# Optimization experiments

Hardware: AMD Instinct MI355X
Metric: run time of the kernel (lower is better)

The kernel has to match this reference:

```python
import jax, jax.numpy as jnp
import numpy as np

N_HEADS = 16

def setup_inputs() -> dict:
    key = jax.random.key(0)
    ks = jax.random.split(key, 9)
    B, S, E = 2, 2048, 1024
    s = 1.0 / np.sqrt(E)
    return {
        "x":  jax.random.normal(ks[0], (B, S, E), jnp.float32),
        "Wq": jax.random.normal(ks[1], (E, E), jnp.float32) * s,
        "bq": jax.random.normal(ks[2], (E,), jnp.float32) * 0.01,
        "Wk": jax.random.normal(ks[3], (E, E), jnp.float32) * s,
        "bk": jax.random.normal(ks[4], (E,), jnp.float32) * 0.01,
        "Wv": jax.random.normal(ks[5], (E, E), jnp.float32) * s,
        "bv": jax.random.normal(ks[6], (E,), jnp.float32) * 0.01,
        "Wo": jax.random.normal(ks[7], (E, E), jnp.float32) * s,
        "bo": jax.random.normal(ks[8], (E,), jnp.float32) * 0.01,
    }

def reference(x, Wq, bq, Wk, bk, Wv, bv, Wo, bo):
    B, S, E = x.shape
    H = N_HEADS
    D = E // H
    # torch nn.Linear: y = x @ W.T + b
    q = (x @ Wq.T + bq).reshape(B, S, H, D)
    k = (x @ Wk.T + bk).reshape(B, S, H, D)
    v = (x @ Wv.T + bv).reshape(B, S, H, D)
    # scores: [B, H, Q, K]
    scores = jnp.einsum('bqnd,bknd->bnqk', q, k) / jnp.sqrt(jnp.float32(D))
    # NOTE: original code softmaxes over dim=1 == the HEADS axis (faithful quirk)
    attn = jax.nn.softmax(scores, axis=1)
    # dropout p=0 -> identity
    out = jnp.einsum('bnqk,bknd->bnqd', attn, v)      # [B, H, Q, D]
    out = out.transpose(0, 2, 1, 3).reshape(B, S, E)  # [B, S, E]
    return out @ Wo.T + bo
```

## Files before the change

### kernel.cpp

```cpp
#include <hip/hip_runtime.h>
#include <cstddef>
#include <cstdint>

#define BATCH 2
#define S_LEN 2048
#define E_DIM 1024
#define NH    16
#define HD    64
#define M_ROWS (BATCH * S_LEN)

#define QSCALE 0.18033688011112042f

typedef unsigned short u16;
typedef short     bf16x8 __attribute__((ext_vector_type(8)));
typedef _Float16  f16x8  __attribute__((ext_vector_type(8)));
typedef __fp16    h16x2  __attribute__((ext_vector_type(2)));
typedef float     f32x4  __attribute__((ext_vector_type(4)));

__device__ __forceinline__ u16 f2bf(float f) {
    union { float f; unsigned u; } v; v.f = f;
    unsigned r = v.u + 0x7fffu + ((v.u >> 16) & 1u);
    return (u16)(r >> 16);
}
__device__ __forceinline__ float bf2f(u16 h) {
    union { unsigned u; float f; } v; v.u = ((unsigned)h) << 16;
    return v.f;
}

__device__ __forceinline__ void load_lds16(const u16* g, u16* l) {
    __builtin_amdgcn_global_load_lds(
        (const __attribute__((address_space(1))) unsigned int*)g,
        (__attribute__((address_space(3))) unsigned int*)l, 16, 0, 0);
}

__global__ void cvt_bf16(const float* __restrict__ in, u16* __restrict__ out, int n)
{
    int i = (blockIdx.x * 256 + threadIdx.x) * 4;
    if (i + 3 < n) {
        float4 v = *(const float4*)(in + i);
        u16 o[4] = { f2bf(v.x), f2bf(v.y), f2bf(v.z), f2bf(v.w) };
        *(uint2*)(out + i) = *(const uint2*)o;
    }
}

__global__ void cvt_w3(const float* __restrict__ Wq, const float* __restrict__ Wk,
                       const float* __restrict__ Wv, u16* __restrict__ out)
{
    const int seg = blockIdx.y;
    const float* src = (seg == 0) ? Wq : (seg == 1) ? Wk : Wv;
    int i = (blockIdx.x * 256 + threadIdx.x) * 4;
    float4 v = *(const float4*)(src + i);
    u16 o[4] = { f2bf(v.x), f2bf(v.y), f2bf(v.z), f2bf(v.w) };
    *(uint2*)(out + (size_t)seg * E_DIM * E_DIM + i) = *(const uint2*)o;
}

__global__ void combine_ctx(const u16* __restrict__ a, const u16* __restrict__ b,
                            u16* __restrict__ c, int n)
{
    int i = (blockIdx.x * 256 + threadIdx.x) * 4;
    if (i + 3 < n) {
        uint2 ua = *(const uint2*)(a + i);
        uint2 ub = *(const uint2*)(b + i);
        const u16* pa = (const u16*)&ua; const u16* pb = (const u16*)&ub;
        u16 o[4];
#pragma unroll
        for (int j = 0; j < 4; ++j) o[j] = f2bf(bf2f(pa[j]) + bf2f(pb[j]));
        *(uint2*)(c + i) = *(const uint2*)o;
    }
}

__global__ __launch_bounds__(256)
void gemm_qkv(const u16* __restrict__ A, const u16* __restrict__ W3,
              const float* __restrict__ bq, const float* __restrict__ bk,
              const float* __restrict__ bv,
              u16* __restrict__ Qb, u16* __restrict__ Kb, u16* __restrict__ Vtb)
{
    __shared__ u16 Al[128 * 32];
    __shared__ u16 Bl[128 * 32];
    const int K = E_DIM;
    const int t = threadIdx.x;
    const int w = t >> 6, lane = t & 63;
    const int quad = lane >> 4, lm = lane & 15;
    const int wy = w >> 1, wx = w & 1;
    const int m0 = blockIdx.x * 128, n0 = blockIdx.y * 128;
    const int lrow  = lane >> 2;
    const int lcol8 = (lane & 3) * 8;

    f32x4 acc[4][4] = {};

    for (int kb = 0; kb < K; kb += 32) {
        __syncthreads();
#pragma unroll
        for (int i = 0; i < 2; ++i) {
            const int r0 = w * 32 + i * 16;
            load_lds16(A  + (size_t)(m0 + r0 + lrow) * K + kb + lcol8, &Al[r0 * 32]);
            load_lds16(W3 + (size_t)(n0 + r0 + lrow) * K + kb + lcol8, &Bl[r0 * 32]);
        }
        __syncthreads();

        bf16x8 af[4], bfr[4];
#pragma unroll
        for (int i = 0; i < 4; ++i)
            af[i] = *(const bf16x8*)(Al + (wy * 64 + i * 16 + lm) * 32 + quad * 8);
#pragma unroll
        for (int j = 0; j < 4; ++j)
            bfr[j] = *(const bf16x8*)(Bl + (wx * 64 + j * 16 + lm) * 32 + quad * 8);
#pragma unroll
        for (int i = 0; i < 4; ++i)
#pragma unroll
            for (int j = 0; j < 4; ++j)
                acc[i][j] = __builtin_amdgcn_mfma_f32_16x16x32_bf16(af[i], bfr[j], acc[i][j], 0, 0, 0);
    }

    const int seg = n0 >> 10;
    const int nl0 = n0 & 1023;
    const float* bs = (seg == 0) ? bq : (seg == 1) ? bk : bv;

    if (seg < 2) {
        u16* dst = (seg == 0) ? Qb : Kb;
        const float scl = (seg == 0) ? QSCALE : 1.0f;
#pragma unroll
        for (int j = 0; j < 4; ++j) {
            const int n = nl0 + wx * 64 + j * 16 + lm;
            const float bias = bs[n];
#pragma unroll
            for (int i = 0; i < 4; ++i) {
                const int mrow = m0 + wy * 64 + i * 16 + quad * 4;
#pragma unroll
                for (int rg = 0; rg < 4; ++rg)
                    dst[(size_t)(mrow + rg) * E_DIM + n] = f2bf((acc[i][j][rg] + bias) * scl);
            }
        }
    } else {
#pragma unroll
        for (int j = 0; j < 4; ++j) {
            const int n = nl0 + wx * 64 + j * 16 + lm;
            const float bias = bs[n];
#pragma unroll
            for (int i = 0; i < 4; ++i) {
                const int mrow = m0 + wy * 64 + i * 16 + quad * 4;
                const int batch = mrow >> 11;
                const int sloc  = mrow & 2047;
                u16 o[4];
#pragma unroll
                for (int rg = 0; rg < 4; ++rg) {
                    union { _Float16 h; u16 u; } cv;
                    cv.h = (_Float16)(acc[i][j][rg] + bias);
                    o[rg] = cv.u;
                }
                *(uint2*)&Vtb[(size_t)batch * E_DIM * S_LEN + (size_t)n * S_LEN + sloc]
                    = *(const uint2*)o;
            }
        }
    }
}

__global__ __launch_bounds__(256)
void gemm_wo(const u16* __restrict__ A, const u16* __restrict__ B,
             const float* __restrict__ bias, float* __restrict__ C)
{
    __shared__ u16 Al[128 * 32];
    __shared__ u16 Bl[128 * 32];
    const int K = E_DIM, N = E_DIM;
    const int t = threadIdx.x;
    const int w = t >> 6, lane = t & 63;
    const int quad = lane >> 4, lm = lane & 15;
    const int wy = w >> 1, wx = w & 1;
    const int m0 = blockIdx.x * 128, n0 = blockIdx.y * 128;
    const int lrow  = lane >> 2;
    const int lcol8 = (lane & 3) * 8;

    f32x4 acc[4][4] = {};

    for (int kb = 0; kb < K; kb += 32) {
        __syncthreads();
#pragma unroll
        for (int i = 0; i < 2; ++i) {
            const int r0 = w * 32 + i * 16;
            load_lds16(A + (size_t)(m0 + r0 + lrow) * K + kb + lcol8, &Al[r0 * 32]);
            load_lds16(B + (size_t)(n0 + r0 + lrow) * K + kb + lcol8, &Bl[r0 * 32]);
        }
        __syncthreads();

        bf16x8 af[4], bfr[4];
#pragma unroll
        for (int i = 0; i < 4; ++i)
            af[i] = *(const bf16x8*)(Al + (wy * 64 + i * 16 + lm) * 32 + quad * 8);
#pragma unroll
        for (int j = 0; j < 4; ++j)
            bfr[j] = *(const bf16x8*)(Bl + (wx * 64 + j * 16 + lm) * 32 + quad * 8);
#pragma unroll
        for (int i = 0; i < 4; ++i)
#pragma unroll
            for (int j = 0; j < 4; ++j)
                acc[i][j] = __builtin_amdgcn_mfma_f32_16x16x32_bf16(af[i], bfr[j], acc[i][j], 0, 0, 0);
    }

#pragma unroll
    for (int j = 0; j < 4; ++j) {
        const int n = n0 + wx * 64 + j * 16 + lm;
        const float bs = bias[n];
#pragma unroll
        for (int i = 0; i < 4; ++i) {
            const int mrow = m0 + wy * 64 + i * 16 + quad * 4;
#pragma unroll
            for (int rg = 0; rg < 4; ++rg)
                C[(size_t)(mrow + rg) * N + n] = acc[i][j][rg] + bs;
        }
    }
}

__global__ __launch_bounds__(512, 2)
void attn_v12(const u16* __restrict__ Q, const u16* __restrict__ K,
              const u16* __restrict__ Vt, u16* __restrict__ ctxA,
              u16* __restrict__ ctxB)
{
    __shared__ __align__(16) u16 smem[38912];
    u16* S4h = smem;
    u16* P5  = smem + 18432;

    const int t     = threadIdx.x;
    const int w     = t >> 6;
    const int lane  = t & 63;
    const int quad  = lane >> 4, lm = lane & 15;

    const int i     = blockIdx.x;
    const int xcd   = i & 7;
    const int combo = xcd >> 1;
    const int b     = combo >> 1;
    const int khalf = combo & 1;
    const int slot  = i >> 3;
    const int qt    = ((xcd & 1) << 5) | slot;
    const int q0    = qt * 32;

    const size_t qbase = ((size_t)b * S_LEN + q0) * E_DIM;
    const size_t kmat  = (size_t)b * S_LEN * E_DIM;
    const size_t vtb   = (size_t)b * E_DIM * S_LEN;

    const int h0 = 2 * w;

    bf16x8 qf[2][2][2];
#pragma unroll
    for (int s = 0; s < 2; ++s)
#pragma unroll
        for (int hp = 0; hp < 2; ++hp)
#pragma unroll
            for (int hf = 0; hf < 2; ++hf)
                qf[s][hp][hf] = *(const bf16x8*)(Q + qbase
                                + (size_t)(s * 16 + lm) * E_DIM
                                + (h0 + hp) * 64 + hf * 32 + quad * 8);

    f32x4 oacc[2][2][4] = {};
    const int kbeg = khalf * (S_LEN / 2);
    const int sq = t & 31, sj = t >> 5;

    for (int c = 0; c < (S_LEN / 2) / 32; ++c) {
        const int k0 = kbeg + c * 32;

        f32x4 sacc[2][2][2];
#pragma unroll
        for (int hp = 0; hp < 2; ++hp)
#pragma unroll
            for (int kt = 0; kt < 2; ++kt) {
                bf16x8 kf0 = *(const bf16x8*)(K + kmat
                             + (size_t)(k0 + kt * 16 + lm) * E_DIM
                             + (h0 + hp) * 64 + quad * 8);
                bf16x8 kf1 = *(const bf16x8*)(K + kmat
                             + (size_t)(k0 + kt * 16 + lm) * E_DIM
                             + (h0 + hp) * 64 + 32 + quad * 8);
#pragma unroll
                for (int s = 0; s < 2; ++s) {
                    f32x4 sf = {};
                    sf = __builtin_amdgcn_mfma_f32_16x16x32_bf16(kf0, qf[s][hp][0], sf, 0, 0, 0);
                    sf = __builtin_amdgcn_mfma_f32_16x16x32_bf16(kf1, qf[s][hp][1], sf, 0, 0, 0);
                    sacc[hp][kt][s] = sf;
                }
            }

#pragma unroll
        for (int kt = 0; kt < 2; ++kt)
#pragma unroll
            for (int s = 0; s < 2; ++s)
#pragma unroll
                for (int rg = 0; rg < 4; ++rg) {
                    union { h16x2 v; unsigned u; } pk;
                    pk.v = __builtin_amdgcn_cvt_pkrtz(sacc[0][kt][s][rg],
                                                      sacc[1][kt][s][rg]);
                    const int kl = kt * 16 + quad * 4 + rg;
                    *(unsigned*)(S4h + (size_t)(kl * 32 + s * 16 + lm) * 18 + 2 * w) = pk.u;
                }

        f16x8 vf[2][4];
#pragma unroll
        for (int hp = 0; hp < 2; ++hp)
#pragma unroll
            for (int dt = 0; dt < 4; ++dt)
                vf[hp][dt] = *(const f16x8*)(Vt + vtb
                             + (size_t)((h0 + hp) * 64 + dt * 16 + lm) * S_LEN
                             + k0 + quad * 8);

        asm volatile("s_waitcnt lgkmcnt(0)" ::: "memory");
        __builtin_amdgcn_s_barrier();

#pragma unroll
        for (int ks = 0; ks < 2; ++ks) {
            const u16* base = S4h + (size_t)((2 * sj + ks) * 32 + sq) * 18;
            union { uint4 u; __fp16 h[8]; } r0, r1;
            r0.u = *(const uint4*)(base);
            r1.u = *(const uint4*)(base + 8);
            float s[16];
#pragma unroll
            for (int z = 0; z < 8; ++z) {
                s[z]     = (float)r0.h[z];
                s[8 + z] = (float)r1.h[z];
            }
            float m = s[0];
#pragma unroll
            for (int h = 1; h < 16; ++h) m = fmaxf(m, s[h]);
            float sum = 0.f;
#pragma unroll
            for (int h = 0; h < 16; ++h) {
                s[h] = __builtin_amdgcn_exp2f(s[h] - m);
                sum += s[h];
            }
            const float inv = __builtin_amdgcn_rcpf(sum);
#pragma unroll
            for (int h = 0; h < 16; ++h) {
                union { __fp16 hv; u16 u; } cv;
                cv.hv = (__fp16)(s[h] * inv);
                P5[(size_t)h * 1280 + sq * 40 + 2 * sj + ks] = cv.u;
            }
        }

        asm volatile("s_waitcnt lgkmcnt(0)" ::: "memory");
        __builtin_amdgcn_s_barrier();

#pragma unroll
        for (int hp = 0; hp < 2; ++hp)
#pragma unroll
            for (int s = 0; s < 2; ++s) {
                f16x8 pa = *(const f16x8*)(P5 + (size_t)(h0 + hp) * 1280
                                           + (s * 16 + lm) * 40 + quad * 8);
#pragma unroll
                for (int dt = 0; dt < 4; ++dt)
                    oacc[hp][s][dt] = __builtin_amdgcn_mfma_f32_16x16x32_f16(
                                          pa, vf[hp][dt], oacc[hp][s][dt], 0, 0, 0);
            }
    }

    __syncthreads();
    u16* Ol = smem;
#pragma unroll
    for (int hp = 0; hp < 2; ++hp) {
        const int h = h0 + hp;
#pragma unroll
        for (int s = 0; s < 2; ++s)
#pragma unroll
            for (int dt = 0; dt < 4; ++dt)
#pragma unroll
                for (int rg = 0; rg < 4; ++rg)
                    Ol[(size_t)(s * 16 + quad * 4 + rg) * 1024 + h * 64 + dt * 16 + lm]
                        = f2bf(oacc[hp][s][dt][rg]);
    }
    __syncthreads();
    u16* dst = khalf ? ctxB : ctxA;
#pragma unroll
    for (int i2 = 0; i2 < 8; ++i2) {
        const int unit = i2 * 512 + t;
        const int r = unit >> 7, cu = unit & 127;
        *(bf16x8*)(dst + ((size_t)b * S_LEN + q0 + r) * E_DIM + cu * 8) =
            *(const bf16x8*)(Ol + (size_t)r * 1024 + cu * 8);
    }
}

extern "C" void kernel_launch(void* const* d_in, const int* in_sizes, int n_in,
                              void* d_out, int out_size, void* d_ws, size_t ws_size,
                              hipStream_t stream)
{
    const float* x  = (const float*)d_in[0];
    const float* Wq = (const float*)d_in[1];
    const float* bq = (const float*)d_in[2];
    const float* Wk = (const float*)d_in[3];
    const float* bk = (const float*)d_in[4];
    const float* Wv = (const float*)d_in[5];
    const float* bv = (const float*)d_in[6];
    const float* Wo = (const float*)d_in[7];
    const float* bo = (const float*)d_in[8];
    float* out = (float*)d_out;

    const size_t MAT = (size_t)M_ROWS * E_DIM;
    const size_t WSZ = (size_t)E_DIM * E_DIM;
    u16* xb   = (u16*)d_ws;
    u16* W3   = xb   + MAT;
    u16* Wob  = W3   + 3 * WSZ;
    u16* Qb   = Wob  + WSZ;
    u16* Kb   = Qb   + MAT;
    u16* Vtb  = Kb   + MAT;
    u16* ctxA = Vtb  + MAT;
    u16* ctxB = ctxA + MAT;

    cvt_bf16<<<(int)(MAT / 1024), 256, 0, stream>>>(x, xb, (int)MAT);
    dim3 wgrid(WSZ / 1024, 3);
    cvt_w3<<<wgrid, 256, 0, stream>>>(Wq, Wk, Wv, W3);
    cvt_bf16<<<(int)(WSZ / 1024), 256, 0, stream>>>(Wo, Wob, (int)WSZ);

    dim3 qkvgrid(M_ROWS / 128, 3 * E_DIM / 128);
    gemm_qkv<<<qkvgrid, 256, 0, stream>>>(xb, W3, bq, bk, bv, Qb, Kb, Vtb);

    attn_v12<<<BATCH * 64 * 2, 512, 0, stream>>>(Qb, Kb, Vtb, ctxA, ctxB);

    combine_ctx<<<(int)(MAT / 1024), 256, 0, stream>>>(ctxA, ctxB, xb, (int)MAT);

    dim3 ogrid(M_ROWS / 128, E_DIM / 128);
    gemm_wo<<<ogrid, 256, 0, stream>>>(xb, Wob, bo, out);
}
```

Before: 333.9 us.

## Process 64-key chunks per barrier pair with swizzled score layout in attention

The attention kernel now handles 64 keys per loop iteration instead of 32, which halves the number of barrier pairs across the key range. Score writes to shared memory use a quad-rotated row index to spread bank accesses. Each thread normalises two key columns and writes packed fp16 pairs to P, and the softmax max and sum use balanced trees. LDS use roughly doubles to about 147KB per block, which leaves room for only one block per CU. The second V fragment load is issued mid-iteration, so its latency may not be hidden.

```diff
diff --git a/kernel.cpp b/kernel.cpp
--- a/kernel.cpp
+++ b/kernel.cpp
@@ -211,13 +211,13 @@
 }
 
 __global__ __launch_bounds__(512, 2)
-void attn_v12(const u16* __restrict__ Q, const u16* __restrict__ K,
+void attn_v13(const u16* __restrict__ Q, const u16* __restrict__ K,
               const u16* __restrict__ Vt, u16* __restrict__ ctxA,
               u16* __restrict__ ctxB)
 {
-    __shared__ __align__(16) u16 smem[38912];
+    __shared__ __align__(16) u16 smem[73728];
     u16* S4h = smem;
-    u16* P5  = smem + 18432;
+    u16* P5  = smem + 36864;
 
     const int t     = threadIdx.x;
     const int w     = t >> 6;
@@ -253,15 +253,16 @@
     f32x4 oacc[2][2][4] = {};
     const int kbeg = khalf * (S_LEN / 2);
     const int sq = t & 31, sj = t >> 5;
-
-    for (int c = 0; c < (S_LEN / 2) / 32; ++c) {
-        const int k0 = kbeg + c * 32;
-
-        f32x4 sacc[2][2][2];
-#pragma unroll
-        for (int hp = 0; hp < 2; ++hp)
-#pragma unroll
-            for (int kt = 0; kt < 2; ++kt) {
+    const int qrot = (sq + 8 * (sj & 3)) & 31;
+
+    for (int c = 0; c < (S_LEN / 2) / 64; ++c) {
+        const int k0 = kbeg + c * 64;
+
+#pragma unroll
+        for (int kt = 0; kt < 4; ++kt) {
+            f32x4 sacc[2][2];
+#pragma unroll
+            for (int hp = 0; hp < 2; ++hp) {
                 bf16x8 kf0 = *(const bf16x8*)(K + kmat
                              + (size_t)(k0 + kt * 16 + lm) * E_DIM
                              + (h0 + hp) * 64 + quad * 8);
@@ -273,22 +274,20 @@
                     f32x4 sf = {};
                     sf = __builtin_amdgcn_mfma_f32_16x16x32_bf16(kf0, qf[s][hp][0], sf, 0, 0, 0);
                     sf = __builtin_amdgcn_mfma_f32_16x16x32_bf16(kf1, qf[s][hp][1], sf, 0, 0, 0);
-                    sacc[hp][kt][s] = sf;
+                    sacc[hp][s] = sf;
                 }
             }
-
-#pragma unroll
-        for (int kt = 0; kt < 2; ++kt)
 #pragma unroll
             for (int s = 0; s < 2; ++s)
 #pragma unroll
                 for (int rg = 0; rg < 4; ++rg) {
                     union { h16x2 v; unsigned u; } pk;
-                    pk.v = __builtin_amdgcn_cvt_pkrtz(sacc[0][kt][s][rg],
-                                                      sacc[1][kt][s][rg]);
-                    const int kl = kt * 16 + quad * 4 + rg;
-                    *(unsigned*)(S4h + (size_t)(kl * 32 + s * 16 + lm) * 18 + 2 * w) = pk.u;
+                    pk.v = __builtin_amdgcn_cvt_pkrtz(sacc[0][s][rg], sacc[1][s][rg]);
+                    const int kl  = kt * 16 + quad * 4 + rg;
+                    const int qph = ((s * 16 + lm) + 8 * quad) & 31;
+                    *(unsigned*)(S4h + (size_t)(kl * 32 + qph) * 18 + 2 * w) = pk.u;
                 }
+        }
 
         f16x8 vf[2][4];
 #pragma unroll
@@ -303,32 +302,46 @@
         __builtin_amdgcn_s_barrier();
 
 #pragma unroll
-        for (int ks = 0; ks < 2; ++ks) {
-            const u16* base = S4h + (size_t)((2 * sj + ks) * 32 + sq) * 18;
-            union { uint4 u; __fp16 h[8]; } r0, r1;
-            r0.u = *(const uint4*)(base);
-            r1.u = *(const uint4*)(base + 8);
-            float s[16];
-#pragma unroll
-            for (int z = 0; z < 8; ++z) {
-                s[z]     = (float)r0.h[z];
-                s[8 + z] = (float)r1.h[z];
-            }
-            float m = s[0];
-#pragma unroll
-            for (int h = 1; h < 16; ++h) m = fmaxf(m, s[h]);
-            float sum = 0.f;
+        for (int p = 0; p < 2; ++p) {
+            float pv0[16], pv1[16];
+#pragma unroll
+            for (int e = 0; e < 2; ++e) {
+                const int k = 4 * sj + 2 * p + e;
+                const u16* base = S4h + (size_t)(k * 32 + qrot) * 18;
+                union { uint4 u; __fp16 h[8]; } r0, r1;
+                r0.u = *(const uint4*)(base);
+                r1.u = *(const uint4*)(base + 8);
+                float s[16];
+#pragma unroll
+                for (int z = 0; z < 8; ++z) {
+                    s[z]     = (float)r0.h[z];
+                    s[8 + z] = (float)r1.h[z];
+                }
+                const float m =
+                    fmaxf(fmaxf(fmaxf(fmaxf(s[0], s[1]), fmaxf(s[2], s[3])),
+                                fmaxf(fmaxf(s[4], s[5]), fmaxf(s[6], s[7]))),
+                          fmaxf(fmaxf(fmaxf(s[8], s[9]), fmaxf(s[10], s[11])),
+                                fmaxf(fmaxf(s[12], s[13]), fmaxf(s[14], s[15]))));
+#pragma unroll
+                for (int h = 0; h < 16; ++h)
+                    s[h] = __builtin_amdgcn_exp2f(s[h] - m);
+                const float sum =
+                    (((s[0] + s[1]) + (s[2] + s[3])) + ((s[4] + s[5]) + (s[6] + s[7]))) +
+                    (((s[8] + s[9]) + (s[10] + s[11])) + ((s[12] + s[13]) + (s[14] + s[15])));
+                const float inv = __builtin_amdgcn_rcpf(sum);
+                if (e == 0) {
+#pragma unroll
+                    for (int h = 0; h < 16; ++h) pv0[h] = s[h] * inv;
+                } else {
+#pragma unroll
+                    for (int h = 0; h < 16; ++h) pv1[h] = s[h] * inv;
+                }
+            }
 #pragma unroll
             for (int h = 0; h < 16; ++h) {
-                s[h] = __builtin_amdgcn_exp2f(s[h] - m);
-                sum += s[h];
-            }
-            const float inv = __builtin_amdgcn_rcpf(sum);
-#pragma unroll
-            for (int h = 0; h < 16; ++h) {
-                union { __fp16 hv; u16 u; } cv;
-                cv.hv = (__fp16)(s[h] * inv);
-                P5[(size_t)h * 1280 + sq * 40 + 2 * sj + ks] = cv.u;
+                union { h16x2 v; unsigned u; } cv;
+                cv.v = __builtin_amdgcn_cvt_pkrtz(pv0[h], pv1[h]);
+                *(unsigned*)(P5 + (size_t)h * 2304 + sq * 72 + 4 * sj + 2 * p) = cv.u;
             }
         }
 
@@ -339,8 +352,28 @@
         for (int hp = 0; hp < 2; ++hp)
 #pragma unroll
             for (int s = 0; s < 2; ++s) {
-                f16x8 pa = *(const f16x8*)(P5 + (size_t)(h0 + hp) * 1280
-                                           + (s * 16 + lm) * 40 + quad * 8);
+                f16x8 pa = *(const f16x8*)(P5 + (size_t)(h0 + hp) * 2304
+                                           + (s * 16 + lm) * 72 + quad * 8);
+#pragma unroll
+                for (int dt = 0; dt < 4; ++dt)
+                    oacc[hp][s][dt] = __builtin_amdgcn_mfma_f32_16x16x32_f16(
+                                          pa, vf[hp][dt], oacc[hp][s][dt], 0, 0, 0);
+            }
+
+#pragma unroll
+        for (int hp = 0; hp < 2; ++hp)
+#pragma unroll
+            for (int dt = 0; dt < 4; ++dt)
+                vf[hp][dt] = *(const f16x8*)(Vt + vtb
+                             + (size_t)((h0 + hp) * 64 + dt * 16 + lm) * S_LEN
+                             + k0 + 32 + quad * 8);
+
+#pragma unroll
+        for (int hp = 0; hp < 2; ++hp)
+#pragma unroll
+            for (int s = 0; s < 2; ++s) {
+                f16x8 pa = *(const f16x8*)(P5 + (size_t)(h0 + hp) * 2304
+                                           + (s * 16 + lm) * 72 + 32 + quad * 8);
 #pragma unroll
                 for (int dt = 0; dt < 4; ++dt)
                     oacc[hp][s][dt] = __builtin_amdgcn_mfma_f32_16x16x32_f16(
@@ -407,7 +440,7 @@
     dim3 qkvgrid(M_ROWS / 128, 3 * E_DIM / 128);
     gemm_qkv<<<qkvgrid, 256, 0, stream>>>(xb, W3, bq, bk, bv, Qb, Kb, Vtb);
 
-    attn_v12<<<BATCH * 64 * 2, 512, 0, stream>>>(Qb, Kb, Vtb, ctxA, ctxB);
+    attn_v13<<<BATCH * 64 * 2, 512, 0, stream>>>(Qb, Kb, Vtb, ctxA, ctxB);
 
     combine_ctx<<<(int)(MAT / 1024), 256, 0, stream>>>(ctxA, ctxB, xb, (int)MAT);
 
```

Measured after the change: 323.4 us. 3.2% less time.

## Assign one head per wave with 1024-thread attention blocks and swizzled score staging

Applied to the files above, without the earlier changes.

The attention kernel moves from 8 waves handling two heads each to 16 waves handling one head each, doubling the threads per block. Each thread now runs one softmax column instead of two. Score stores are scalar fp16 with a rotated query index to cut LDS bank conflicts, and the max and sum reductions are written as trees. This trades fewer registers per thread and more parallelism for more barrier participants and smaller, scalar LDS writes.

```diff
diff --git a/kernel.cpp b/kernel.cpp
--- a/kernel.cpp
+++ b/kernel.cpp
@@ -25,6 +25,9 @@
 __device__ __forceinline__ float bf2f(u16 h) {
     union { unsigned u; float f; } v; v.u = ((unsigned)h) << 16;
     return v.f;
+}
+__device__ __forceinline__ u16 f2h(float f) {
+    union { __fp16 h; u16 u; } cv; cv.h = (__fp16)f; return cv.u;
 }
 
 __device__ __forceinline__ void load_lds16(const u16* g, u16* l) {
@@ -210,8 +213,8 @@
     }
 }
 
-__global__ __launch_bounds__(512, 2)
-void attn_v12(const u16* __restrict__ Q, const u16* __restrict__ K,
+__global__ __launch_bounds__(1024, 4)
+void attn_v15(const u16* __restrict__ Q, const u16* __restrict__ K,
               const u16* __restrict__ Vt, u16* __restrict__ ctxA,
               u16* __restrict__ ctxB)
 {
@@ -223,6 +226,7 @@
     const int w     = t >> 6;
     const int lane  = t & 63;
     const int quad  = lane >> 4, lm = lane & 15;
+    const int h     = w;
 
     const int i     = blockIdx.x;
     const int xcd   = i & 7;
@@ -237,136 +241,116 @@
     const size_t kmat  = (size_t)b * S_LEN * E_DIM;
     const size_t vtb   = (size_t)b * E_DIM * S_LEN;
 
-    const int h0 = 2 * w;
-
-    bf16x8 qf[2][2][2];
+    bf16x8 qf[2][2];
 #pragma unroll
     for (int s = 0; s < 2; ++s)
 #pragma unroll
-        for (int hp = 0; hp < 2; ++hp)
-#pragma unroll
-            for (int hf = 0; hf < 2; ++hf)
-                qf[s][hp][hf] = *(const bf16x8*)(Q + qbase
-                                + (size_t)(s * 16 + lm) * E_DIM
-                                + (h0 + hp) * 64 + hf * 32 + quad * 8);
-
-    f32x4 oacc[2][2][4] = {};
+        for (int hf = 0; hf < 2; ++hf)
+            qf[s][hf] = *(const bf16x8*)(Q + qbase
+                        + (size_t)(s * 16 + lm) * E_DIM
+                        + h * 64 + hf * 32 + quad * 8);
+
+    f32x4 oacc[2][4] = {};
     const int kbeg = khalf * (S_LEN / 2);
-    const int sq = t & 31, sj = t >> 5;
+    const int sq = t & 31, sk = t >> 5;
+    const int qrot = (sq + 8 * ((sk >> 2) & 3)) & 31;
 
     for (int c = 0; c < (S_LEN / 2) / 32; ++c) {
         const int k0 = kbeg + c * 32;
 
-        f32x4 sacc[2][2][2];
-#pragma unroll
-        for (int hp = 0; hp < 2; ++hp)
-#pragma unroll
-            for (int kt = 0; kt < 2; ++kt) {
-                bf16x8 kf0 = *(const bf16x8*)(K + kmat
-                             + (size_t)(k0 + kt * 16 + lm) * E_DIM
-                             + (h0 + hp) * 64 + quad * 8);
-                bf16x8 kf1 = *(const bf16x8*)(K + kmat
-                             + (size_t)(k0 + kt * 16 + lm) * E_DIM
-                             + (h0 + hp) * 64 + 32 + quad * 8);
-#pragma unroll
-                for (int s = 0; s < 2; ++s) {
-                    f32x4 sf = {};
-                    sf = __builtin_amdgcn_mfma_f32_16x16x32_bf16(kf0, qf[s][hp][0], sf, 0, 0, 0);
-                    sf = __builtin_amdgcn_mfma_f32_16x16x32_bf16(kf1, qf[s][hp][1], sf, 0, 0, 0);
-                    sacc[hp][kt][s] = sf;
+#pragma unroll
+        for (int kt = 0; kt < 2; ++kt) {
+            bf16x8 kf0 = *(const bf16x8*)(K + kmat
+                         + (size_t)(k0 + kt * 16 + lm) * E_DIM
+                         + h * 64 + quad * 8);
+            bf16x8 kf1 = *(const bf16x8*)(K + kmat
+                         + (size_t)(k0 + kt * 16 + lm) * E_DIM
+                         + h * 64 + 32 + quad * 8);
+            f32x4 sacc[2];
+#pragma unroll
+            for (int s = 0; s < 2; ++s) {
+                f32x4 sf = {};
+                sf = __builtin_amdgcn_mfma_f32_16x16x32_bf16(kf0, qf[s][0], sf, 0, 0, 0);
+                sf = __builtin_amdgcn_mfma_f32_16x16x32_bf16(kf1, qf[s][1], sf, 0, 0, 0);
+                sacc[s] = sf;
+            }
+#pragma unroll
+            for (int s = 0; s < 2; ++s)
+#pragma unroll
+                for (int rg = 0; rg < 4; ++rg) {
+                    const int kl  = kt * 16 + quad * 4 + rg;
+                    const int qph = ((s * 16 + lm) + 8 * quad) & 31;
+                    S4h[(size_t)(kl * 32 + qph) * 18 + h] = f2h(sacc[s][rg]);
                 }
-            }
-
-#pragma unroll
-        for (int kt = 0; kt < 2; ++kt)
-#pragma unroll
-            for (int s = 0; s < 2; ++s)
-#pragma unroll
-                for (int rg = 0; rg < 4; ++rg) {
-                    union { h16x2 v; unsigned u; } pk;
-                    pk.v = __builtin_amdgcn_cvt_pkrtz(sacc[0][kt][s][rg],
-                                                      sacc[1][kt][s][rg]);
-                    const int kl = kt * 16 + quad * 4 + rg;
-                    *(unsigned*)(S4h + (size_t)(kl * 32 + s * 16 + lm) * 18 + 2 * w) = pk.u;
-                }
-
-        f16x8 vf[2][4];
-#pragma unroll
-        for (int hp = 0; hp < 2; ++hp)
-#pragma unroll
-            for (int dt = 0; dt < 4; ++dt)
-                vf[hp][dt] = *(const f16x8*)(Vt + vtb
-                             + (size_t)((h0 + hp) * 64 + dt * 16 + lm) * S_LEN
-                             + k0 + quad * 8);
+        }
+
+        f16x8 vf[4];
+#pragma unroll
+        for (int dt = 0; dt < 4; ++dt)
+            vf[dt] = *(const f16x8*)(Vt + vtb
+                     + (size_t)(h * 64 + dt * 16 + lm) * S_LEN
+                     + k0 + quad * 8);
 
         asm volatile("s_waitcnt lgkmcnt(0)" ::: "memory");
         __builtin_amdgcn_s_barrier();
 
-#pragma unroll
-        for (int ks = 0; ks < 2; ++ks) {
-            const u16* base = S4h + (size_t)((2 * sj + ks) * 32 + sq) * 18;
-            union { uint4 u; __fp16 h[8]; } r0, r1;
+        {
+            const u16* base = S4h + (size_t)(sk * 32 + qrot) * 18;
+            union { uint4 u; __fp16 hh[8]; } r0, r1;
             r0.u = *(const uint4*)(base);
             r1.u = *(const uint4*)(base + 8);
             float s[16];
 #pragma unroll
             for (int z = 0; z < 8; ++z) {
-                s[z]     = (float)r0.h[z];
-                s[8 + z] = (float)r1.h[z];
+                s[z]     = (float)r0.hh[z];
+                s[8 + z] = (float)r1.hh[z];
             }
-            float m = s[0];
-#pragma unroll
-            for (int h = 1; h < 16; ++h) m = fmaxf(m, s[h]);
-            float sum = 0.f;
-#pragma unroll
-            for (int h = 0; h < 16; ++h) {
-                s[h] = __builtin_amdgcn_exp2f(s[h] - m);
-                sum += s[h];
-            }
+            const float m =
+                fmaxf(fmaxf(fmaxf(fmaxf(s[0], s[1]), fmaxf(s[2], s[3])),
+                            fmaxf(fmaxf(s[4], s[5]), fmaxf(s[6], s[7]))),
+                      fmaxf(fmaxf(fmaxf(s[8], s[9]), fmaxf(s[10], s[11])),
+                            fmaxf(fmaxf(s[12], s[13]), fmaxf(s[14], s[15]))));
+#pragma unroll
+            for (int hh = 0; hh < 16; ++hh)
+                s[hh] = __builtin_amdgcn_exp2f(s[hh] - m);
+            const float sum =
+                (((s[0] + s[1]) + (s[2] + s[3])) + ((s[4] + s[5]) + (s[6] + s[7]))) +
+                (((s[8] + s[9]) + (s[10] + s[11])) + ((s[12] + s[13]) + (s[14] + s[15])));
             const float inv = __builtin_amdgcn_rcpf(sum);
 #pragma unroll
-            for (int h = 0; h < 16; ++h) {
-                union { __fp16 hv; u16 u; } cv;
-                cv.hv = (__fp16)(s[h] * inv);
-                P5[(size_t)h * 1280 + sq * 40 + 2 * sj + ks] = cv.u;
-            }
+            for (int hh = 0; hh < 16; ++hh)
+                P5[(size_t)hh * 1280 + sq * 40 + sk] = f2h(s[hh] * inv);
         }
 
         asm volatile("s_waitcnt lgkmcnt(0)" ::: "memory");
         __builtin_amdgcn_s_barrier();
 
 #pragma unroll
-        for (int hp = 0; hp < 2; ++hp)
-#pragma unroll
-            for (int s = 0; s < 2; ++s) {
-                f16x8 pa = *(const f16x8*)(P5 + (size_t)(h0 + hp) * 1280
-                                           + (s * 16 + lm) * 40 + quad * 8);
-#pragma unroll
-                for (int dt = 0; dt < 4; ++dt)
-                    oacc[hp][s][dt] = __builtin_amdgcn_mfma_f32_16x16x32_f16(
-                                          pa, vf[hp][dt], oacc[hp][s][dt], 0, 0, 0);
-            }
+        for (int s = 0; s < 2; ++s) {
+            f16x8 pa = *(const f16x8*)(P5 + (size_t)h * 1280
+                                       + (s * 16 + lm) * 40 + quad * 8);
+#pragma unroll
+            for (int dt = 0; dt < 4; ++dt)
+                oacc[s][dt] = __builtin_amdgcn_mfma_f32_16x16x32_f16(
+                                  pa, vf[dt], oacc[s][dt], 0, 0, 0);
+        }
     }
 
     __syncthreads();
     u16* Ol = smem;
 #pragma unroll
-    for (int hp = 0; hp < 2; ++hp) {
-        const int h = h0 + hp;
-#pragma unroll
-        for (int s = 0; s < 2; ++s)
-#pragma unroll
-            for (int dt = 0; dt < 4; ++dt)
-#pragma unroll
-                for (int rg = 0; rg < 4; ++rg)
-                    Ol[(size_t)(s * 16 + quad * 4 + rg) * 1024 + h * 64 + dt * 16 + lm]
-                        = f2bf(oacc[hp][s][dt][rg]);
-    }
+    for (int s = 0; s < 2; ++s)
+#pragma unroll
+        for (int dt = 0; dt < 4; ++dt)
+#pragma unroll
+            for (int rg = 0; rg < 4; ++rg)
+                Ol[(size_t)(s * 16 + quad * 4 + rg) * 1024 + h * 64 + dt * 16 + lm]
+                    = f2bf(oacc[s][dt][rg]);
     __syncthreads();
     u16* dst = khalf ? ctxB : ctxA;
 #pragma unroll
-    for (int i2 = 0; i2 < 8; ++i2) {
-        const int unit = i2 * 512 + t;
+    for (int i2 = 0; i2 < 4; ++i2) {
+        const int unit = i2 * 1024 + t;
         const int r = unit >> 7, cu = unit & 127;
         *(bf16x8*)(dst + ((size_t)b * S_LEN + q0 + r) * E_DIM + cu * 8) =
             *(const bf16x8*)(Ol + (size_t)r * 1024 + cu * 8);
@@ -407,7 +391,7 @@
     dim3 qkvgrid(M_ROWS / 128, 3 * E_DIM / 128);
     gemm_qkv<<<qkvgrid, 256, 0, stream>>>(xb, W3, bq, bk, bv, Qb, Kb, Vtb);
 
-    attn_v12<<<BATCH * 64 * 2, 512, 0, stream>>>(Qb, Kb, Vtb, ctxA, ctxB);
+    attn_v15<<<BATCH * 64 * 2, 1024, 0, stream>>>(Qb, Kb, Vtb, ctxA, ctxB);
 
     combine_ctx<<<(int)(MAT / 1024), 256, 0, stream>>>(ctxA, ctxB, xb, (int)MAT);
 
```

New measurement: 343.1 us. 1.03x slower.

## Software-pipeline attention stages with double-buffered LDS and one barrier per chunk

Applied to the files above, without the earlier changes.

Restructures the attention loop into a three-stage software pipeline (QK^T, cross-head softmax, PV) working on different key chunks at once. It double-buffers the score and probability LDS tiles so only one barrier is needed per iteration instead of two. It also rotates the score row index to cut LDS bank conflicts, and packs two probabilities per 32-bit store. The cost is double the shared memory (about 152 KB), which may limit occupancy below the declared two blocks per CU, plus higher register pressure.

```diff
diff --git a/kernel.cpp b/kernel.cpp
--- a/kernel.cpp
+++ b/kernel.cpp
@@ -210,14 +210,113 @@
     }
 }
 
+#define QKT_ST(S4W, KOFF)                                                     \
+  _Pragma("unroll")                                                           \
+  for (int kt = 0; kt < 2; ++kt) {                                            \
+    f32x4 sacc_[2][2];                                                        \
+    _Pragma("unroll")                                                         \
+    for (int hp = 0; hp < 2; ++hp) {                                          \
+      bf16x8 kf0_ = *(const bf16x8*)(K + kmat                                 \
+                    + (size_t)((KOFF) + kt * 16 + lm) * E_DIM                 \
+                    + (h0 + hp) * 64 + quad * 8);                             \
+      bf16x8 kf1_ = *(const bf16x8*)(K + kmat                                 \
+                    + (size_t)((KOFF) + kt * 16 + lm) * E_DIM                 \
+                    + (h0 + hp) * 64 + 32 + quad * 8);                        \
+      _Pragma("unroll")                                                       \
+      for (int s = 0; s < 2; ++s) {                                           \
+        f32x4 sf_ = {};                                                       \
+        sf_ = __builtin_amdgcn_mfma_f32_16x16x32_bf16(kf0_, qf[s][hp][0], sf_, 0, 0, 0); \
+        sf_ = __builtin_amdgcn_mfma_f32_16x16x32_bf16(kf1_, qf[s][hp][1], sf_, 0, 0, 0); \
+        sacc_[hp][s] = sf_;                                                   \
+      }                                                                       \
+    }                                                                         \
+    _Pragma("unroll")                                                         \
+    for (int s = 0; s < 2; ++s)                                               \
+      _Pragma("unroll")                                                       \
+      for (int rg = 0; rg < 4; ++rg) {                                        \
+        union { h16x2 v; unsigned u; } pk_;                                   \
+        pk_.v = __builtin_amdgcn_cvt_pkrtz(sacc_[0][s][rg], sacc_[1][s][rg]); \
+        const int kl_  = kt * 16 + quad * 4 + rg;                             \
+        const int qph_ = ((s * 16 + lm) + 8 * quad) & 31;                     \
+        *(unsigned*)((S4W) + (size_t)(kl_ * 32 + qph_) * 18 + 2 * w) = pk_.u; \
+      }                                                                       \
+  }
+
+#define SM_ST(S4R, P5W)                                                       \
+  {                                                                           \
+    float pv0[16], pv1[16];                                                   \
+    _Pragma("unroll")                                                         \
+    for (int e = 0; e < 2; ++e) {                                             \
+      const int kk_ = 2 * sj + e;                                             \
+      const u16* base_ = (S4R) + (size_t)(kk_ * 32 + qrot) * 18;              \
+      union { uint4 u; __fp16 hh[8]; } r0_, r1_;                              \
+      r0_.u = *(const uint4*)(base_);                                         \
+      r1_.u = *(const uint4*)(base_ + 8);                                     \
+      float s_[16];                                                           \
+      _Pragma("unroll")                                                       \
+      for (int z = 0; z < 8; ++z) {                                           \
+        s_[z] = (float)r0_.hh[z]; s_[8 + z] = (float)r1_.hh[z];               \
+      }                                                                       \
+      const float m_ =                                                        \
+          fmaxf(fmaxf(fmaxf(fmaxf(s_[0], s_[1]), fmaxf(s_[2], s_[3])),        \
+                      fmaxf(fmaxf(s_[4], s_[5]), fmaxf(s_[6], s_[7]))),       \
+                fmaxf(fmaxf(fmaxf(s_[8], s_[9]), fmaxf(s_[10], s_[11])),      \
+                      fmaxf(fmaxf(s_[12], s_[13]), fmaxf(s_[14], s_[15])))); \
+      _Pragma("unroll")                                                       \
+      for (int hh = 0; hh < 16; ++hh)                                         \
+        s_[hh] = __builtin_amdgcn_exp2f(s_[hh] - m_);                         \
+      const float sum_ =                                                      \
+          (((s_[0] + s_[1]) + (s_[2] + s_[3])) + ((s_[4] + s_[5]) + (s_[6] + s_[7]))) + \
+          (((s_[8] + s_[9]) + (s_[10] + s_[11])) + ((s_[12] + s_[13]) + (s_[14] + s_[15]))); \
+      const float inv_ = __builtin_amdgcn_rcpf(sum_);                         \
+      if (e == 0) {                                                           \
+        _Pragma("unroll")                                                     \
+        for (int hh = 0; hh < 16; ++hh) pv0[hh] = s_[hh] * inv_;              \
+      } else {                                                                \
+        _Pragma("unroll")                                                     \
+        for (int hh = 0; hh < 16; ++hh) pv1[hh] = s_[hh] * inv_;              \
+      }                                                                       \
+    }                                                                         \
+    _Pragma("unroll")                                                         \
+    for (int hh = 0; hh < 16; ++hh) {                                         \
+      union { h16x2 v; unsigned u; } cv_;                                     \
+      cv_.v = __builtin_amdgcn_cvt_pkrtz(pv0[hh], pv1[hh]);                   \
+      *(unsigned*)((P5W) + (size_t)hh * 1280 + sq * 40 + 2 * sj) = cv_.u;     \
+    }                                                                         \
+  }
+
+#define V_ST(KOFF)                                                            \
+  _Pragma("unroll")                                                           \
+  for (int hp = 0; hp < 2; ++hp)                                              \
+    _Pragma("unroll")                                                         \
+    for (int dt = 0; dt < 4; ++dt)                                            \
+      vf[hp][dt] = *(const f16x8*)(Vt + vtb                                   \
+                   + (size_t)((h0 + hp) * 64 + dt * 16 + lm) * S_LEN          \
+                   + (KOFF) + quad * 8);
+
+#define PV_ST(P5R)                                                            \
+  _Pragma("unroll")                                                           \
+  for (int hp = 0; hp < 2; ++hp)                                              \
+    _Pragma("unroll")                                                         \
+    for (int s = 0; s < 2; ++s) {                                             \
+      f16x8 pa_ = *(const f16x8*)((P5R) + (size_t)(h0 + hp) * 1280            \
+                                  + (s * 16 + lm) * 40 + quad * 8);           \
+      _Pragma("unroll")                                                       \
+      for (int dt = 0; dt < 4; ++dt)                                          \
+        oacc[hp][s][dt] = __builtin_amdgcn_mfma_f32_16x16x32_f16(             \
+                              pa_, vf[hp][dt], oacc[hp][s][dt], 0, 0, 0);     \
+    }
+
+#define PHASE_END                                                             \
+  asm volatile("s_waitcnt lgkmcnt(0)" ::: "memory");                          \
+  __builtin_amdgcn_s_barrier();
+
 __global__ __launch_bounds__(512, 2)
-void attn_v12(const u16* __restrict__ Q, const u16* __restrict__ K,
+void attn_v16(const u16* __restrict__ Q, const u16* __restrict__ K,
               const u16* __restrict__ Vt, u16* __restrict__ ctxA,
               u16* __restrict__ ctxB)
 {
-    __shared__ __align__(16) u16 smem[38912];
-    u16* S4h = smem;
-    u16* P5  = smem + 18432;
+    __shared__ __align__(16) u16 smem[77824];
 
     const int t     = threadIdx.x;
     const int w     = t >> 6;
@@ -251,102 +350,40 @@
                                 + (h0 + hp) * 64 + hf * 32 + quad * 8);
 
     f32x4 oacc[2][2][4] = {};
+    f16x8 vf[2][4];
     const int kbeg = khalf * (S_LEN / 2);
     const int sq = t & 31, sj = t >> 5;
-
-    for (int c = 0; c < (S_LEN / 2) / 32; ++c) {
-        const int k0 = kbeg + c * 32;
-
-        f32x4 sacc[2][2][2];
-#pragma unroll
-        for (int hp = 0; hp < 2; ++hp)
-#pragma unroll
-            for (int kt = 0; kt < 2; ++kt) {
-                bf16x8 kf0 = *(const bf16x8*)(K + kmat
-                             + (size_t)(k0 + kt * 16 + lm) * E_DIM
-                             + (h0 + hp) * 64 + quad * 8);
-                bf16x8 kf1 = *(const bf16x8*)(K + kmat
-                             + (size_t)(k0 + kt * 16 + lm) * E_DIM
-                             + (h0 + hp) * 64 + 32 + quad * 8);
-#pragma unroll
-                for (int s = 0; s < 2; ++s) {
-                    f32x4 sf = {};
-                    sf = __builtin_amdgcn_mfma_f32_16x16x32_bf16(kf0, qf[s][hp][0], sf, 0, 0, 0);
-                    sf = __builtin_amdgcn_mfma_f32_16x16x32_bf16(kf1, qf[s][hp][1], sf, 0, 0, 0);
-                    sacc[hp][kt][s] = sf;
-                }
-            }
-
-#pragma unroll
-        for (int kt = 0; kt < 2; ++kt)
-#pragma unroll
-            for (int s = 0; s < 2; ++s)
-#pragma unroll
-                for (int rg = 0; rg < 4; ++rg) {
-                    union { h16x2 v; unsigned u; } pk;
-                    pk.v = __builtin_amdgcn_cvt_pkrtz(sacc[0][kt][s][rg],
-                                                      sacc[1][kt][s][rg]);
-                    const int kl = kt * 16 + quad * 4 + rg;
-                    *(unsigned*)(S4h + (size_t)(kl * 32 + s * 16 + lm) * 18 + 2 * w) = pk.u;
-                }
-
-        f16x8 vf[2][4];
-#pragma unroll
-        for (int hp = 0; hp < 2; ++hp)
-#pragma unroll
-            for (int dt = 0; dt < 4; ++dt)
-                vf[hp][dt] = *(const f16x8*)(Vt + vtb
-                             + (size_t)((h0 + hp) * 64 + dt * 16 + lm) * S_LEN
-                             + k0 + quad * 8);
-
-        asm volatile("s_waitcnt lgkmcnt(0)" ::: "memory");
-        __builtin_amdgcn_s_barrier();
-
-#pragma unroll
-        for (int ks = 0; ks < 2; ++ks) {
-            const u16* base = S4h + (size_t)((2 * sj + ks) * 32 + sq) * 18;
-            union { uint4 u; __fp16 h[8]; } r0, r1;
-            r0.u = *(const uint4*)(base);
-            r1.u = *(const uint4*)(base + 8);
-            float s[16];
-#pragma unroll
-            for (int z = 0; z < 8; ++z) {
-                s[z]     = (float)r0.h[z];
-                s[8 + z] = (float)r1.h[z];
-            }
-            float m = s[0];
-#pragma unroll
-            for (int h = 1; h < 16; ++h) m = fmaxf(m, s[h]);
-            float sum = 0.f;
-#pragma unroll
-            for (int h = 0; h < 16; ++h) {
-                s[h] = __builtin_amdgcn_exp2f(s[h] - m);
-                sum += s[h];
-            }
-            const float inv = __builtin_amdgcn_rcpf(sum);
-#pragma unroll
-            for (int h = 0; h < 16; ++h) {
-                union { __fp16 hv; u16 u; } cv;
-                cv.hv = (__fp16)(s[h] * inv);
-                P5[(size_t)h * 1280 + sq * 40 + 2 * sj + ks] = cv.u;
-            }
-        }
-
-        asm volatile("s_waitcnt lgkmcnt(0)" ::: "memory");
-        __builtin_amdgcn_s_barrier();
-
-#pragma unroll
-        for (int hp = 0; hp < 2; ++hp)
-#pragma unroll
-            for (int s = 0; s < 2; ++s) {
-                f16x8 pa = *(const f16x8*)(P5 + (size_t)(h0 + hp) * 1280
-                                           + (s * 16 + lm) * 40 + quad * 8);
-#pragma unroll
-                for (int dt = 0; dt < 4; ++dt)
-                    oacc[hp][s][dt] = __builtin_amdgcn_mfma_f32_16x16x32_f16(
-                                          pa, vf[hp][dt], oacc[hp][s][dt], 0, 0, 0);
-            }
-    }
+    const int qrot = (sq + 8 * ((sj >> 1) & 3)) & 31;
+
+    u16* const S4_0 = smem;
+    u16* const S4_1 = smem + 18432;
+    u16* const P5_0 = smem + 36864;
+    u16* const P5_1 = smem + 57344;
+
+    QKT_ST(S4_0, kbeg)
+    PHASE_END
+    QKT_ST(S4_1, kbeg + 32)
+    SM_ST (S4_0, P5_0)
+    PHASE_END
+
+    for (int c = 2; c < 32; ++c) {
+        u16* S4w = (c & 1) ? S4_1 : S4_0;
+        u16* S4r = (c & 1) ? S4_0 : S4_1;
+        u16* P5w = (c & 1) ? P5_0 : P5_1;
+        u16* P5r = (c & 1) ? P5_1 : P5_0;
+        V_ST  (kbeg + (c - 2) * 32)
+        QKT_ST(S4w, kbeg + c * 32)
+        SM_ST (S4r, P5w)
+        PV_ST (P5r)
+        PHASE_END
+    }
+
+    V_ST  (kbeg + 30 * 32)
+    SM_ST (S4_1, P5_1)
+    PV_ST (P5_0)
+    PHASE_END
+    V_ST  (kbeg + 31 * 32)
+    PV_ST (P5_1)
 
     __syncthreads();
     u16* Ol = smem;
@@ -372,6 +409,12 @@
             *(const bf16x8*)(Ol + (size_t)r * 1024 + cu * 8);
     }
 }
+
+#undef QKT_ST
+#undef SM_ST
+#undef V_ST
+#undef PV_ST
+#undef PHASE_END
 
 extern "C" void kernel_launch(void* const* d_in, const int* in_sizes, int n_in,
                               void* d_out, int out_size, void* d_ws, size_t ws_size,
@@ -407,7 +450,7 @@
     dim3 qkvgrid(M_ROWS / 128, 3 * E_DIM / 128);
     gemm_qkv<<<qkvgrid, 256, 0, stream>>>(xb, W3, bq, bk, bv, Qb, Kb, Vtb);
 
-    attn_v12<<<BATCH * 64 * 2, 512, 0, stream>>>(Qb, Kb, Vtb, ctxA, ctxB);
+    attn_v16<<<BATCH * 64 * 2, 512, 0, stream>>>(Qb, Kb, Vtb, ctxA, ctxB);
 
     combine_ctx<<<(int)(MAT / 1024), 256, 0, stream>>>(ctxA, ctxB, xb, (int)MAT);
 
```

New measurement: 298.0 us. -10.7%, faster.
